# Kernel tuning notes

Hardware: AMD Instinct MI355X
Metric: run time of the kernel (lower is better)

Reference implementation:

```python
import jax, jax.numpy as jnp
import numpy as np

N, E = 50000, 800000
IN_DIM, HID, OUT_DIM = 128, 64, 64
H1, H2 = 4, 2
LRELU_SLOPE = 0.2
LN_EPS = 1e-5


def _glorot(key, shape):
    fan = shape[0] + shape[-1]
    lim = float(np.sqrt(6.0 / fan))
    return jax.random.uniform(key, shape, jnp.float32, -lim, lim)


def setup_inputs() -> dict:
    key = jax.random.key(0)
    ks = jax.random.split(key, 12)
    x = jax.random.normal(ks[0], (N, IN_DIM), jnp.float32)
    edge_index = jax.random.randint(ks[1], (2, E), 0, N, jnp.int64)
    return {
        "x": x,
        "edge_index": edge_index,
        # layer 1: GATConv(128 -> 64, heads=4, concat=True)
        "W1": _glorot(ks[2], (IN_DIM, H1 * HID)),
        "att_src1": _glorot(ks[3], (H1, HID)),
        "att_dst1": _glorot(ks[4], (H1, HID)),
        "b1": jnp.zeros((H1 * HID,), jnp.float32),
        # LayerNorm(256)
        "ln_w": jnp.ones((H1 * HID,), jnp.float32),
        "ln_b": jnp.zeros((H1 * HID,), jnp.float32),
        # layer 2: GATConv(256 -> 64, heads=2, concat=False)
        "W2": _glorot(ks[5], (H1 * HID, H2 * OUT_DIM)),
        "att_src2": _glorot(ks[6], (H2, OUT_DIM)),
        "att_dst2": _glorot(ks[7], (H2, OUT_DIM)),
        "b2": jnp.zeros((OUT_DIM,), jnp.float32),
    }


def gat_layer(x, src, dst, W, a_src, a_dst, bias, heads, out_ch, concat):
    n = x.shape[0]
    h = (x @ W).reshape(n, heads, out_ch)                 # [N,H,C]
    al_s = jnp.einsum("nhc,hc->nh", h, a_src)             # [N,H]
    al_d = jnp.einsum("nhc,hc->nh", h, a_dst)
    e = jax.nn.leaky_relu(al_s[src] + al_d[dst], LRELU_SLOPE)  # [E,H]
    # segment softmax over incoming edges of each dst node
    m = jax.ops.segment_max(e, dst, num_segments=n)
    e = jnp.exp(e - m[dst])
    denom = jax.ops.segment_sum(e, dst, num_segments=n)
    alpha = e / denom[dst]                                # [E,H]
    msg = h[src] * alpha[:, :, None]                      # [E,H,C]
    out = jax.ops.segment_sum(msg, dst, num_segments=n)   # [N,H,C]
    out = out.reshape(n, heads * out_ch) if concat else out.mean(axis=1)
    return out + bias


def layer_norm(x, w, b):
    mu = x.mean(axis=-1, keepdims=True)
    var = ((x - mu) ** 2).mean(axis=-1, keepdims=True)
    return (x - mu) * jax.lax.rsqrt(var + LN_EPS) * w + b


def reference(x, edge_index, W1, att_src1, att_dst1, b1, ln_w, ln_b,
              W2, att_src2, att_dst2, b2):
    # PyG GATConv adds self-loops by default
    loops = jnp.arange(N, dtype=edge_index.dtype)
    src = jnp.concatenate([edge_index[0], loops])
    dst = jnp.concatenate([edge_index[1], loops])
    h = gat_layer(x, src, dst, W1, att_src1, att_dst1, b1, H1, HID, True)
    h = layer_norm(h, ln_w, ln_b)
    h = jax.nn.elu(h)
    # dropout is identity in eval mode
    h = gat_layer(h, src, dst, W2, att_src2, att_dst2, b2, H2, OUT_DIM, False)
    return h
```

## Files before the change

### kernel.cpp

```cpp
#include <hip/hip_runtime.h>
#include <hip/hip_bf16.h>
#include <math.h>

#define IN_DIM  128
#define HID     64
#define H1      4
#define H2      2
#define OUT_DIM 64
#define D1      256
#define D2      128
#define LRELU   0.2f
#define LN_EPS  1e-5f
#define BK      16
#define NS      8
#define HKPS    49
#define MAXNB   4096

using short8 = __attribute__((ext_vector_type(8))) short;
using f32x4  = __attribute__((ext_vector_type(4))) float;

static __device__ __forceinline__ unsigned short f2bf_bits(float f)
{
    __hip_bfloat16 b = __float2bfloat16(f);
    return *reinterpret_cast<unsigned short*>(&b);
}
static __device__ __forceinline__ float2 unpack_bf2(unsigned int p)
{
    float2 r;
    r.x = __uint_as_float(p << 16);
    r.y = __uint_as_float(p & 0xffff0000u);
    return r;
}
static __device__ __forceinline__ unsigned int pack_bf2(float x, float y)
{
    return (unsigned int)f2bf_bits(x) | ((unsigned int)f2bf_bits(y) << 16);
}

static __device__ __forceinline__ float lrelu_exp(float v)
{
    v = v > 0.f ? v : LRELU * v;
    return __expf(v);
}

static __device__ __forceinline__ int detect_i64(const int* __restrict__ ei)
{
    int any_odd_nonzero = 0;
    #pragma unroll
    for (int k = 1; k < 16; k += 2) any_odd_nonzero |= (ei[k] != 0);
    return any_odd_nonzero ? 0 : 1;
}

__global__ __launch_bounds__(256) void conv_hist_kernel(
    const float* __restrict__ W1, const float* __restrict__ W2,
    unsigned short* __restrict__ Wp1, unsigned short* __restrict__ Wp2,
    const int* __restrict__ ei, int E, int* __restrict__ sdeg, int NB)
{
    __shared__ int hist[MAXNB];
    const int bid = blockIdx.x;
    if (bid < 256) {
        int tid = bid * 256 + threadIdx.x;
        if (tid < 32768) {
            int j = tid & 7, l = (tid >> 3) & 63, rest = tid >> 9;
            int s = rest & 15, t = rest >> 4;
            int k = t * 32 + (l >> 4) * 8 + j, col = s * 16 + (l & 15);
            Wp1[tid] = f2bf_bits(W1[k * D1 + col]);
        } else {
            int id = tid - 32768;
            int j = id & 7, l = (id >> 3) & 63, rest = id >> 9;
            int s = rest & 7, t = rest >> 3;
            int k = t * 32 + (l >> 4) * 8 + j, col = s * 16 + (l & 15);
            Wp2[id] = f2bf_bits(W2[k * D2 + col]);
        }
        return;
    }

    const int i64f = detect_i64(ei);
    const int h = bid - 256;
    const int s = h & 7, k = h >> 3;
    const int numGroups = (E + 255) >> 8;

    for (int i = threadIdx.x; i < NB; i += 256) hist[i] = 0;
    __syncthreads();

    for (int g = s + 8 * k; g < numGroups; g += 8 * HKPS) {
        int e = (g << 8) + threadIdx.x;
        if (e < E) {
            int dst = i64f ? ei[2 * ((size_t)E + e)] : ei[E + e];
            atomicAdd(&hist[dst >> 4], 1);
        }
    }
    __syncthreads();
    for (int i = threadIdx.x; i < NB; i += 256) {
        int v = hist[i];
        if (v) atomicAdd(&sdeg[s * NB + i], v);
    }
}

__global__ __launch_bounds__(256) void scan_gemm1_kernel(
    const int* __restrict__ sdeg, int NB, int M, int* __restrict__ bsum, int scanB,
    const float* __restrict__ x, const unsigned short* __restrict__ Wp,
    const float* __restrict__ att_s, const float* __restrict__ att_d,
    unsigned short* __restrict__ h1b,
    float* __restrict__ al_s, float* __restrict__ al_d, int N)
{
    __shared__ __align__(16) unsigned short As[16 * 136];
    const int tid = threadIdx.x;

    if ((int)blockIdx.x < scanB) {
        int* sh = (int*)As;
        int i = blockIdx.x * 256 + tid;
        int v = 0;
        if (i < M) v = sdeg[(i & 7) * NB + (i >> 3)];
        sh[tid] = v;
        __syncthreads();
        for (int st = 128; st > 0; st >>= 1) {
            if (tid < st) sh[tid] += sh[tid + st];
            __syncthreads();
        }
        if (tid == 0) bsum[blockIdx.x] = sh[0];
        return;
    }

    const int n0 = ((int)blockIdx.x - scanB) * 16;
    const int l = tid & 63, w = tid >> 6;

    #pragma unroll
    for (int it = 0; it < 2; ++it) {
        int ch = tid + it * 256;
        int r = ch >> 5, c4 = (ch & 31) * 4;
        int row = n0 + r;
        float4 v = (row < N) ? ((const float4*)x)[(size_t)row * 32 + (c4 >> 2)]
                             : make_float4(0.f, 0.f, 0.f, 0.f);
        ushort4 pk = make_ushort4(f2bf_bits(v.x), f2bf_bits(v.y),
                                  f2bf_bits(v.z), f2bf_bits(v.w));
        *(ushort4*)&As[r * 136 + c4] = pk;
    }

    short8 bfr[4][4];
    #pragma unroll
    for (int t = 0; t < 4; ++t)
        #pragma unroll
        for (int p = 0; p < 4; ++p)
            bfr[t][p] = ((const short8*)Wp)[(t * 16 + (w * 4 + p)) * 64 + l];

    __syncthreads();

    f32x4 acc[4] = {{0.f,0.f,0.f,0.f},{0.f,0.f,0.f,0.f},
                    {0.f,0.f,0.f,0.f},{0.f,0.f,0.f,0.f}};
    #pragma unroll
    for (int t = 0; t < 4; ++t) {
        short8 a = *(const short8*)&As[(l & 15) * 136 + t * 32 + (l >> 4) * 8];
        #pragma unroll
        for (int p = 0; p < 4; ++p)
            acc[p] = __builtin_amdgcn_mfma_f32_16x16x32_bf16(a, bfr[t][p], acc[p], 0, 0, 0);
    }

    const int colbase = w * 64 + (l & 15);
    const int rowbase = n0 + (l >> 4) * 4;
    #pragma unroll
    for (int p = 0; p < 4; ++p) {
        int col = colbase + p * 16;
        #pragma unroll
        for (int r = 0; r < 4; ++r) {
            int row = rowbase + r;
            if (row < N) h1b[(size_t)row * D1 + col] = f2bf_bits(acc[p][r]);
        }
    }

    float as_p[4], ad_p[4];
    #pragma unroll
    for (int p = 0; p < 4; ++p) {
        as_p[p] = att_s[colbase + p * 16];
        ad_p[p] = att_d[colbase + p * 16];
    }
    #pragma unroll
    for (int r = 0; r < 4; ++r) {
        float ps = acc[0][r] * as_p[0] + acc[1][r] * as_p[1]
                 + acc[2][r] * as_p[2] + acc[3][r] * as_p[3];
        float pd = acc[0][r] * ad_p[0] + acc[1][r] * ad_p[1]
                 + acc[2][r] * ad_p[2] + acc[3][r] * ad_p[3];
        #pragma unroll
        for (int off = 8; off > 0; off >>= 1) {
            ps += __shfl_down(ps, off);
            pd += __shfl_down(pd, off);
        }
        int row = rowbase + r;
        if ((l & 15) == 0 && row < N) {
            al_s[(size_t)row * H1 + w] = ps;
            al_d[(size_t)row * H1 + w] = pd;
        }
    }
}

__global__ __launch_bounds__(256) void scan_final(
    const int* __restrict__ sdeg, const int* __restrict__ bsum, int B, int M, int NB,
    int* __restrict__ start, int* __restrict__ bcur)
{
    __shared__ int sb[256];
    __shared__ int s[256];
    sb[threadIdx.x] = (threadIdx.x < B) ? bsum[threadIdx.x] : 0;
    __syncthreads();
    for (int st = 1; st < 256; st <<= 1) {
        int t = (threadIdx.x >= st) ? sb[threadIdx.x - st] : 0;
        __syncthreads();
        sb[threadIdx.x] += t;
        __syncthreads();
    }
    const int blockOff = (blockIdx.x == 0) ? 0 : sb[blockIdx.x - 1];

    int i = blockIdx.x * 256 + threadIdx.x;
    int v = (i < M) ? sdeg[(i & 7) * NB + (i >> 3)] : 0;
    s[threadIdx.x] = v;
    __syncthreads();
    for (int st = 1; st < 256; st <<= 1) {
        int t = (threadIdx.x >= st) ? s[threadIdx.x - st] : 0;
        __syncthreads();
        s[threadIdx.x] += t;
        __syncthreads();
    }
    int excl = s[threadIdx.x] - v + blockOff;
    if (i < M) {
        start[i] = excl;
        bcur[(i & 7) * NB + (i >> 3)] = excl;
    }
}

__global__ __launch_bounds__(256) void bucket_scatter(
    const int* __restrict__ ei, int E, int NB,
    int* __restrict__ bcur, unsigned int* __restrict__ pairs)
{
    const int i64f = detect_i64(ei);
    int e = blockIdx.x * 256 + threadIdx.x;
    if (e >= E) return;
    int src, dst;
    if (i64f) { src = ei[2 * (size_t)e]; dst = ei[2 * ((size_t)E + e)]; }
    else      { src = ei[e];             dst = ei[E + e]; }
    int s = (e >> 8) & 7;
    int pos = atomicAdd(&bcur[s * NB + (dst >> 4)], 1);
    pairs[pos] = ((unsigned int)src << 16) | (unsigned int)dst;
}

__global__ __launch_bounds__(256) void fill2_kernel(
    const unsigned int* __restrict__ pairs, const int* __restrict__ start,
    int N, int NB, int E,
    int* __restrict__ rowptr, int* __restrict__ csr_src)
{
    __shared__ int cnt[BK], cur[BK];
    __shared__ int stage[2048];
    const int b = blockIdx.x;
    const int t = threadIdx.x;
    const int base = start[b * 8];
    const int segend = (b + 1 < NB) ? start[(b + 1) * 8] : E;
    const int seglen = segend - base;

    if (t < BK) cnt[t] = 0;
    __syncthreads();
    for (int i = t; i < seglen; i += 256)
        atomicAdd(&cnt[pairs[base + i] & (BK - 1)], 1);
    __syncthreads();
    if (t == 0) {
        int run = 0;
        for (int j = 0; j < BK; ++j) {
            cur[j] = run;
            int node = b * BK + j;
            if (node < N) rowptr[node] = base + run;
            run += cnt[j];
        }
        if (b == NB - 1) rowptr[N] = E;
    }
    __syncthreads();

    if (seglen <= 2048) {
        for (int i = t; i < seglen; i += 256) {
            unsigned int p = pairs[base + i];
            int pos = atomicAdd(&cur[p & (BK - 1)], 1);
            stage[pos] = (int)(p >> 16);
        }
        __syncthreads();
        for (int i = t; i < seglen; i += 256)
            csr_src[base + i] = stage[i];
    } else {
        for (int i = t; i < seglen; i += 256) {
            unsigned int p = pairs[base + i];
            int pos = atomicAdd(&cur[p & (BK - 1)], 1);
            csr_src[base + pos] = (int)(p >> 16);
        }
    }
}

__global__ __launch_bounds__(256) void gemm2_mfma(
    const unsigned short* __restrict__ hmidb, const unsigned short* __restrict__ Wp,
    const float* __restrict__ att_s, const float* __restrict__ att_d,
    unsigned short* __restrict__ h2b,
    float* __restrict__ al_s, float* __restrict__ al_d, int N)
{
    __shared__ __align__(16) unsigned short As[16 * 264];
    __shared__ float psL[4][16], pdL[4][16];
    const int tid = threadIdx.x;
    const int n0 = blockIdx.x * 16;
    const int l = tid & 63, w = tid >> 6;

    const short8 zero8 = {0,0,0,0,0,0,0,0};
    #pragma unroll
    for (int it = 0; it < 2; ++it) {
        int ch = tid + it * 256;
        int r = ch >> 5, c8 = (ch & 31) * 8;
        int row = n0 + r;
        short8 v = (row < N) ? ((const short8*)hmidb)[(size_t)row * 32 + (ch & 31)] : zero8;
        *(short8*)&As[r * 264 + c8] = v;
    }

    short8 bfr[8][2];
    #pragma unroll
    for (int t = 0; t < 8; ++t)
        #pragma unroll
        for (int q = 0; q < 2; ++q)
            bfr[t][q] = ((const short8*)Wp)[(t * 8 + (w * 2 + q)) * 64 + l];

    __syncthreads();

    f32x4 acc[2] = {{0.f,0.f,0.f,0.f},{0.f,0.f,0.f,0.f}};
    #pragma unroll
    for (int t = 0; t < 8; ++t) {
        short8 a = *(const short8*)&As[(l & 15) * 264 + t * 32 + (l >> 4) * 8];
        #pragma unroll
        for (int q = 0; q < 2; ++q)
            acc[q] = __builtin_amdgcn_mfma_f32_16x16x32_bf16(a, bfr[t][q], acc[q], 0, 0, 0);
    }

    const int colbase = w * 32 + (l & 15);
    const int rowbase = n0 + (l >> 4) * 4;
    #pragma unroll
    for (int q = 0; q < 2; ++q) {
        int col = colbase + q * 16;
        #pragma unroll
        for (int r = 0; r < 4; ++r) {
            int row = rowbase + r;
            if (row < N) h2b[(size_t)row * D2 + col] = f2bf_bits(acc[q][r]);
        }
    }

    float as_q[2], ad_q[2];
    #pragma unroll
    for (int q = 0; q < 2; ++q) {
        as_q[q] = att_s[colbase + q * 16];
        ad_q[q] = att_d[colbase + q * 16];
    }
    #pragma unroll
    for (int r = 0; r < 4; ++r) {
        float ps = acc[0][r] * as_q[0] + acc[1][r] * as_q[1];
        float pd = acc[0][r] * ad_q[0] + acc[1][r] * ad_q[1];
        #pragma unroll
        for (int off = 8; off > 0; off >>= 1) {
            ps += __shfl_down(ps, off);
            pd += __shfl_down(pd, off);
        }
        if ((l & 15) == 0) {
            psL[w][(l >> 4) * 4 + r] = ps;
            pdL[w][(l >> 4) * 4 + r] = pd;
        }
    }
    __syncthreads();
    if (tid < 32) {
        int rl = tid & 15, hh = tid >> 4;
        int row = n0 + rl;
        if (row < N) {
            al_s[(size_t)row * H2 + hh] = psL[2*hh][rl] + psL[2*hh+1][rl];
            al_d[(size_t)row * H2 + hh] = pdL[2*hh][rl] + pdL[2*hh+1][rl];
        }
    }
}

__global__ __launch_bounds__(64) void agg1_kernel(
    const int* __restrict__ rowptr, const int* __restrict__ csr_src,
    const uint2* __restrict__ h1p,
    const float* __restrict__ al_s, const float* __restrict__ al_d,
    const float* __restrict__ b1,
    const float* __restrict__ ln_w, const float* __restrict__ ln_b,
    uint2* __restrict__ hmidp, int N)
{
    const int n = blockIdx.x;
    const int l = threadIdx.x;
    const int h = l >> 4;
    const float ad = al_d[(size_t)n * H1 + h];

    float a0[4] = {0.f,0.f,0.f,0.f}, a1[4] = {0.f,0.f,0.f,0.f};
    float a2[4] = {0.f,0.f,0.f,0.f}, a3[4] = {0.f,0.f,0.f,0.f};
    float dn0, dn1 = 0.f, dn2 = 0.f, dn3 = 0.f;

    {
        float w = lrelu_exp(al_s[(size_t)n * H1 + h] + ad);
        uint2 p = h1p[(size_t)n * 64 + l];
        float2 va = unpack_bf2(p.x), vb = unpack_bf2(p.y);
        a0[0] = w * va.x; a0[1] = w * va.y; a0[2] = w * vb.x; a0[3] = w * vb.y;
        dn0 = w;
    }

    const int beg = rowptr[n], end = rowptr[n + 1];
    int i = beg;

#define LOADI(k)  int s##k = csr_src[i + k];
#define LOADR(k)  uint2 p##k = h1p[(size_t)s##k * 64 + l]; \
                  float g##k = al_s[(size_t)s##k * H1 + h];
#define WACC(A, D, k) { float w = lrelu_exp(g##k + ad); \
                        float2 va = unpack_bf2(p##k.x), vb = unpack_bf2(p##k.y); \
                        A[0] += w * va.x; A[1] += w * va.y; \
                        A[2] += w * vb.x; A[3] += w * vb.y; D += w; }

    for (; i + 4 <= end; i += 4) {
        LOADI(0) LOADI(1) LOADI(2) LOADI(3)
        LOADR(0) LOADR(1) LOADR(2) LOADR(3)
        WACC(a0, dn0, 0) WACC(a1, dn1, 1) WACC(a2, dn2, 2) WACC(a3, dn3, 3)
    }
    for (; i < end; ++i) {
        LOADI(0) LOADR(0) WACC(a0, dn0, 0)
    }
#undef LOADI
#undef LOADR
#undef WACC

    const float inv = 1.f / ((dn0 + dn1) + (dn2 + dn3));
    float4 bb = ((const float4*)b1)[l];
    float v[4];
    v[0] = ((a0[0]+a1[0]) + (a2[0]+a3[0])) * inv + bb.x;
    v[1] = ((a0[1]+a1[1]) + (a2[1]+a3[1])) * inv + bb.y;
    v[2] = ((a0[2]+a1[2]) + (a2[2]+a3[2])) * inv + bb.z;
    v[3] = ((a0[3]+a1[3]) + (a2[3]+a3[3])) * inv + bb.w;

    float s  = (v[0]+v[1]) + (v[2]+v[3]);
    float s2 = (v[0]*v[0]+v[1]*v[1]) + (v[2]*v[2]+v[3]*v[3]);
    #pragma unroll
    for (int off = 32; off > 0; off >>= 1) {
        s  += __shfl_down(s,  off);
        s2 += __shfl_down(s2, off);
    }
    const float mu   = __shfl(s,  0) * (1.f / 256.f);
    const float ex2  = __shfl(s2, 0) * (1.f / 256.f);
    const float rstd = rsqrtf(ex2 - mu * mu + LN_EPS);
    float4 lw = ((const float4*)ln_w)[l];
    float4 lb = ((const float4*)ln_b)[l];
    float y0 = (v[0] - mu) * rstd * lw.x + lb.x;
    float y1 = (v[1] - mu) * rstd * lw.y + lb.y;
    float y2 = (v[2] - mu) * rstd * lw.z + lb.z;
    float y3 = (v[3] - mu) * rstd * lw.w + lb.w;
    y0 = y0 > 0.f ? y0 : (__expf(y0) - 1.f);
    y1 = y1 > 0.f ? y1 : (__expf(y1) - 1.f);
    y2 = y2 > 0.f ? y2 : (__expf(y2) - 1.f);
    y3 = y3 > 0.f ? y3 : (__expf(y3) - 1.f);
    uint2 outp;
    outp.x = pack_bf2(y0, y1);
    outp.y = pack_bf2(y2, y3);
    hmidp[(size_t)n * 64 + l] = outp;
}

__global__ __launch_bounds__(64) void agg2_kernel(
    const int* __restrict__ rowptr, const int* __restrict__ csr_src,
    const unsigned int* __restrict__ h2p,
    const float* __restrict__ al_s, const float* __restrict__ al_d,
    const float* __restrict__ b2,
    float* __restrict__ out, int N)
{
    const int n = blockIdx.x;
    const int l = threadIdx.x;
    const int h = l >> 5;
    const float ad = al_d[(size_t)n * H2 + h];

    float ax0, ay0, dn0;
    float ax1 = 0.f, ay1 = 0.f, dn1 = 0.f;
    float ax2 = 0.f, ay2 = 0.f, dn2 = 0.f;
    float ax3 = 0.f, ay3 = 0.f, dn3 = 0.f;
    {
        float w = lrelu_exp(al_s[(size_t)n * H2 + h] + ad);
        float2 hv = unpack_bf2(h2p[(size_t)n * 64 + l]);
        ax0 = w * hv.x; ay0 = w * hv.y; dn0 = w;
    }

    const int beg = rowptr[n], end = rowptr[n + 1];
    int i = beg;

#define LOADI(k)  int s##k = csr_src[i + k];
#define LOADR(k)  unsigned int p##k = h2p[(size_t)s##k * 64 + l]; \
                  float g##k = al_s[(size_t)s##k * H2 + h];
#define WACC(AX, AY, D, k) { float w = lrelu_exp(g##k + ad); \
                             float2 vv = unpack_bf2(p##k); \
                             AX += w * vv.x; AY += w * vv.y; D += w; }

    for (; i + 4 <= end; i += 4) {
        LOADI(0) LOADI(1) LOADI(2) LOADI(3)
        LOADR(0) LOADR(1) LOADR(2) LOADR(3)
        WACC(ax0, ay0, dn0, 0) WACC(ax1, ay1, dn1, 1)
        WACC(ax2, ay2, dn2, 2) WACC(ax3, ay3, dn3, 3)
    }
    for (; i < end; ++i) {
        LOADI(0) LOADR(0) WACC(ax0, ay0, dn0, 0)
    }
#undef LOADI
#undef LOADR
#undef WACC

    const float inv = 1.f / ((dn0 + dn1) + (dn2 + dn3));
    const float vx = ((ax0 + ax1) + (ax2 + ax3)) * inv;
    const float vy = ((ay0 + ay1) + (ay2 + ay3)) * inv;

    const float vx1 = __shfl(vx, l + 32);
    const float vy1 = __shfl(vy, l + 32);
    if (l < 32) {
        float2 bb = ((const float2*)b2)[l];
        float2 o;
        o.x = 0.5f * (vx + vx1) + bb.x;
        o.y = 0.5f * (vy + vy1) + bb.y;
        ((float2*)out)[(size_t)n * 32 + l] = o;
    }
}

extern "C" void kernel_launch(void* const* d_in, const int* in_sizes, int n_in,
                              void* d_out, int out_size, void* d_ws, size_t ws_size,
                              hipStream_t stream)
{
    const float* x   = (const float*)d_in[0];
    const int*   ei  = (const int*)d_in[1];
    const float* W1  = (const float*)d_in[2];
    const float* as1 = (const float*)d_in[3];
    const float* ad1 = (const float*)d_in[4];
    const float* b1  = (const float*)d_in[5];
    const float* lnw = (const float*)d_in[6];
    const float* lnb = (const float*)d_in[7];
    const float* W2  = (const float*)d_in[8];
    const float* as2 = (const float*)d_in[9];
    const float* ad2 = (const float*)d_in[10];
    const float* b2  = (const float*)d_in[11];

    const int N = in_sizes[0] / IN_DIM;
    const int E = in_sizes[1] / 2;
    const int NB = (N + BK - 1) / BK;
    const int M  = NB * NS;

    char* ws = (char*)d_ws;
    const size_t szH1b = (size_t)N * D1 * sizeof(unsigned short);
    unsigned short* h1b   = (unsigned short*)(ws);
    unsigned short* hmidb = (unsigned short*)(ws + szH1b);
    unsigned short* Wp1   = (unsigned short*)(ws + 2 * szH1b);
    unsigned short* Wp2   = Wp1 + 32768;
    float* al_s1 = (float*)(Wp2 + 32768);
    float* al_d1 = al_s1 + (size_t)N * H1;
    float* al_s2 = al_d1 + (size_t)N * H1;
    float* al_d2 = al_s2 + (size_t)N * H2;
    int* sdeg    = (int*)(al_d2 + (size_t)N * H2);
    int* bcur    = sdeg + M;
    int* start   = bcur + M;
    int* rowptr  = start + M;
    int* csr_src = rowptr + (N + 1);
    int* bsum    = csr_src + E;
    unsigned int* pairs = (unsigned int*)(bsum + 256);
    unsigned short* h2b = h1b;

    hipMemsetAsync(sdeg, 0, (size_t)M * sizeof(int), stream);

    const int edgeBlocks = (E + 255) / 256;
    const int scanBlocks = (M + 255) / 256;
    const int tileBlocks = (N + 15) / 16;

    conv_hist_kernel<<<256 + NS * HKPS, 256, 0, stream>>>(W1, W2, Wp1, Wp2, ei, E, sdeg, NB);
    scan_gemm1_kernel<<<scanBlocks + tileBlocks, 256, 0, stream>>>(
        sdeg, NB, M, bsum, scanBlocks, x, Wp1, as1, ad1, h1b, al_s1, al_d1, N);
    scan_final<<<scanBlocks, 256, 0, stream>>>(sdeg, bsum, scanBlocks, M, NB, start, bcur);
    bucket_scatter<<<edgeBlocks, 256, 0, stream>>>(ei, E, NB, bcur, pairs);
    fill2_kernel<<<NB, 256, 0, stream>>>(pairs, start, N, NB, E, rowptr, csr_src);

    agg1_kernel<<<N, 64, 0, stream>>>(rowptr, csr_src, (const uint2*)h1b,
                                      al_s1, al_d1, b1, lnw, lnb,
                                      (uint2*)hmidb, N);
    gemm2_mfma<<<tileBlocks, 256, 0, stream>>>(hmidb, Wp2, as2, ad2, h2b, al_s2, al_d2, N);
    agg2_kernel<<<N, 64, 0, stream>>>(rowptr, csr_src, (const unsigned int*)h2b,
                                      al_s2, al_d2, b2, (float*)d_out, N);
}
```

Before: 275.0 us.

## Use 64 per-block histogram slices with direct stores instead of atomics

The dst histogram now gives each of 64 blocks its own slice, written with plain stores. This removes the global atomics and the memset of sdeg. The bucket scatter spreads edges over 64 sub-slices, which cuts atomic contention on the bucket cursors. The scan and final scan are reworked for the larger M: block offsets are now computed by reducing the preceding block sums instead of a 256-entry scan. The cost is a larger M to scan, and only 64 blocks reading all edges during the histogram phase, which may be underparallel.

```diff
diff --git a/kernel.cpp b/kernel.cpp
--- a/kernel.cpp
+++ b/kernel.cpp
@@ -12,8 +12,7 @@
 #define LRELU   0.2f
 #define LN_EPS  1e-5f
 #define BK      16
-#define NS      8
-#define HKPS    49
+#define NSS     64
 #define MAXNB   4096
 
 using short8 = __attribute__((ext_vector_type(8))) short;
@@ -75,14 +74,13 @@
     }
 
     const int i64f = detect_i64(ei);
-    const int h = bid - 256;
-    const int s = h & 7, k = h >> 3;
+    const int s = bid - 256;
     const int numGroups = (E + 255) >> 8;
 
     for (int i = threadIdx.x; i < NB; i += 256) hist[i] = 0;
     __syncthreads();
 
-    for (int g = s + 8 * k; g < numGroups; g += 8 * HKPS) {
+    for (int g = s; g < numGroups; g += NSS) {
         int e = (g << 8) + threadIdx.x;
         if (e < E) {
             int dst = i64f ? ei[2 * ((size_t)E + e)] : ei[E + e];
@@ -90,10 +88,8 @@
         }
     }
     __syncthreads();
-    for (int i = threadIdx.x; i < NB; i += 256) {
-        int v = hist[i];
-        if (v) atomicAdd(&sdeg[s * NB + i], v);
-    }
+    for (int i = threadIdx.x; i < NB; i += 256)
+        sdeg[s * NB + i] = hist[i];
 }
 
 __global__ __launch_bounds__(256) void scan_gemm1_kernel(
@@ -110,7 +106,7 @@
         int* sh = (int*)As;
         int i = blockIdx.x * 256 + tid;
         int v = 0;
-        if (i < M) v = sdeg[(i & 7) * NB + (i >> 3)];
+        if (i < M) v = sdeg[(i & 63) * NB + (i >> 6)];
         sh[tid] = v;
         __syncthreads();
         for (int st = 128; st > 0; st >>= 1) {
@@ -193,23 +189,23 @@
 }
 
 __global__ __launch_bounds__(256) void scan_final(
-    const int* __restrict__ sdeg, const int* __restrict__ bsum, int B, int M, int NB,
+    const int* __restrict__ sdeg, const int* __restrict__ bsum, int M, int NB,
     int* __restrict__ start, int* __restrict__ bcur)
 {
-    __shared__ int sb[256];
+    __shared__ int red[256];
     __shared__ int s[256];
-    sb[threadIdx.x] = (threadIdx.x < B) ? bsum[threadIdx.x] : 0;
-    __syncthreads();
-    for (int st = 1; st < 256; st <<= 1) {
-        int t = (threadIdx.x >= st) ? sb[threadIdx.x - st] : 0;
+    int part = 0;
+    for (int j = threadIdx.x; j < (int)blockIdx.x; j += 256) part += bsum[j];
+    red[threadIdx.x] = part;
+    __syncthreads();
+    for (int st = 128; st > 0; st >>= 1) {
+        if (threadIdx.x < st) red[threadIdx.x] += red[threadIdx.x + st];
         __syncthreads();
-        sb[threadIdx.x] += t;
-        __syncthreads();
-    }
-    const int blockOff = (blockIdx.x == 0) ? 0 : sb[blockIdx.x - 1];
+    }
+    const int blockOff = red[0];
 
     int i = blockIdx.x * 256 + threadIdx.x;
-    int v = (i < M) ? sdeg[(i & 7) * NB + (i >> 3)] : 0;
+    int v = (i < M) ? sdeg[(i & 63) * NB + (i >> 6)] : 0;
     s[threadIdx.x] = v;
     __syncthreads();
     for (int st = 1; st < 256; st <<= 1) {
@@ -221,7 +217,7 @@
     int excl = s[threadIdx.x] - v + blockOff;
     if (i < M) {
         start[i] = excl;
-        bcur[(i & 7) * NB + (i >> 3)] = excl;
+        bcur[(i & 63) * NB + (i >> 6)] = excl;
     }
 }
 
@@ -235,7 +231,7 @@
     int src, dst;
     if (i64f) { src = ei[2 * (size_t)e]; dst = ei[2 * ((size_t)E + e)]; }
     else      { src = ei[e];             dst = ei[E + e]; }
-    int s = (e >> 8) & 7;
+    int s = (e >> 8) & 63;
     int pos = atomicAdd(&bcur[s * NB + (dst >> 4)], 1);
     pairs[pos] = ((unsigned int)src << 16) | (unsigned int)dst;
 }
@@ -249,8 +245,8 @@
     __shared__ int stage[2048];
     const int b = blockIdx.x;
     const int t = threadIdx.x;
-    const int base = start[b * 8];
-    const int segend = (b + 1 < NB) ? start[(b + 1) * 8] : E;
+    const int base = start[b * NSS];
+    const int segend = (b + 1 < NB) ? start[(b + 1) * NSS] : E;
     const int seglen = segend - base;
 
     if (t < BK) cnt[t] = 0;
@@ -533,7 +529,7 @@
     const int N = in_sizes[0] / IN_DIM;
     const int E = in_sizes[1] / 2;
     const int NB = (N + BK - 1) / BK;
-    const int M  = NB * NS;
+    const int M  = NB * NSS;
 
     char* ws = (char*)d_ws;
     const size_t szH1b = (size_t)N * D1 * sizeof(unsigned short);
@@ -551,19 +547,17 @@
     int* rowptr  = start + M;
     int* csr_src = rowptr + (N + 1);
     int* bsum    = csr_src + E;
-    unsigned int* pairs = (unsigned int*)(bsum + 256);
+    unsigned int* pairs = (unsigned int*)(bsum + 1024);
     unsigned short* h2b = h1b;
-
-    hipMemsetAsync(sdeg, 0, (size_t)M * sizeof(int), stream);
 
     const int edgeBlocks = (E + 255) / 256;
     const int scanBlocks = (M + 255) / 256;
     const int tileBlocks = (N + 15) / 16;
 
-    conv_hist_kernel<<<256 + NS * HKPS, 256, 0, stream>>>(W1, W2, Wp1, Wp2, ei, E, sdeg, NB);
+    conv_hist_kernel<<<256 + NSS, 256, 0, stream>>>(W1, W2, Wp1, Wp2, ei, E, sdeg, NB);
     scan_gemm1_kernel<<<scanBlocks + tileBlocks, 256, 0, stream>>>(
         sdeg, NB, M, bsum, scanBlocks, x, Wp1, as1, ad1, h1b, al_s1, al_d1, N);
-    scan_final<<<scanBlocks, 256, 0, stream>>>(sdeg, bsum, scanBlocks, M, NB, start, bcur);
+    scan_final<<<scanBlocks, 256, 0, stream>>>(sdeg, bsum, M, NB, start, bcur);
     bucket_scatter<<<edgeBlocks, 256, 0, stream>>>(ei, E, NB, bcur, pairs);
     fill2_kernel<<<NB, 256, 0, stream>>>(pairs, start, N, NB, E, rowptr, csr_src);
 
```

Result: slower. 285.6 us (+3.8%).

## Fuse CSR fill with layer-1 aggregation, reading neighbor lists from shared memory

Applied to the files above, without the earlier changes.

The CSR bucket fill and the layer-1 attention aggregation now run in one kernel. After building each 16-node bucket's sorted source list in shared memory, the block's four waves each aggregate four nodes straight from that staged list. This removes one kernel launch and the global re-read of rowptr and csr_src for layer 1. In exchange, each block is serialized over 16 nodes with only 4 waves, which could lower parallelism and latency hiding compared with the previous one-wave-per-node grid.

```diff
diff --git a/kernel.cpp b/kernel.cpp
--- a/kernel.cpp
+++ b/kernel.cpp
@@ -240,147 +240,14 @@
     pairs[pos] = ((unsigned int)src << 16) | (unsigned int)dst;
 }
 
-__global__ __launch_bounds__(256) void fill2_kernel(
-    const unsigned int* __restrict__ pairs, const int* __restrict__ start,
-    int N, int NB, int E,
-    int* __restrict__ rowptr, int* __restrict__ csr_src)
-{
-    __shared__ int cnt[BK], cur[BK];
-    __shared__ int stage[2048];
-    const int b = blockIdx.x;
-    const int t = threadIdx.x;
-    const int base = start[b * 8];
-    const int segend = (b + 1 < NB) ? start[(b + 1) * 8] : E;
-    const int seglen = segend - base;
-
-    if (t < BK) cnt[t] = 0;
-    __syncthreads();
-    for (int i = t; i < seglen; i += 256)
-        atomicAdd(&cnt[pairs[base + i] & (BK - 1)], 1);
-    __syncthreads();
-    if (t == 0) {
-        int run = 0;
-        for (int j = 0; j < BK; ++j) {
-            cur[j] = run;
-            int node = b * BK + j;
-            if (node < N) rowptr[node] = base + run;
-            run += cnt[j];
-        }
-        if (b == NB - 1) rowptr[N] = E;
-    }
-    __syncthreads();
-
-    if (seglen <= 2048) {
-        for (int i = t; i < seglen; i += 256) {
-            unsigned int p = pairs[base + i];
-            int pos = atomicAdd(&cur[p & (BK - 1)], 1);
-            stage[pos] = (int)(p >> 16);
-        }
-        __syncthreads();
-        for (int i = t; i < seglen; i += 256)
-            csr_src[base + i] = stage[i];
-    } else {
-        for (int i = t; i < seglen; i += 256) {
-            unsigned int p = pairs[base + i];
-            int pos = atomicAdd(&cur[p & (BK - 1)], 1);
-            csr_src[base + pos] = (int)(p >> 16);
-        }
-    }
-}
-
-__global__ __launch_bounds__(256) void gemm2_mfma(
-    const unsigned short* __restrict__ hmidb, const unsigned short* __restrict__ Wp,
-    const float* __restrict__ att_s, const float* __restrict__ att_d,
-    unsigned short* __restrict__ h2b,
-    float* __restrict__ al_s, float* __restrict__ al_d, int N)
-{
-    __shared__ __align__(16) unsigned short As[16 * 264];
-    __shared__ float psL[4][16], pdL[4][16];
-    const int tid = threadIdx.x;
-    const int n0 = blockIdx.x * 16;
-    const int l = tid & 63, w = tid >> 6;
-
-    const short8 zero8 = {0,0,0,0,0,0,0,0};
-    #pragma unroll
-    for (int it = 0; it < 2; ++it) {
-        int ch = tid + it * 256;
-        int r = ch >> 5, c8 = (ch & 31) * 8;
-        int row = n0 + r;
-        short8 v = (row < N) ? ((const short8*)hmidb)[(size_t)row * 32 + (ch & 31)] : zero8;
-        *(short8*)&As[r * 264 + c8] = v;
-    }
-
-    short8 bfr[8][2];
-    #pragma unroll
-    for (int t = 0; t < 8; ++t)
-        #pragma unroll
-        for (int q = 0; q < 2; ++q)
-            bfr[t][q] = ((const short8*)Wp)[(t * 8 + (w * 2 + q)) * 64 + l];
-
-    __syncthreads();
-
-    f32x4 acc[2] = {{0.f,0.f,0.f,0.f},{0.f,0.f,0.f,0.f}};
-    #pragma unroll
-    for (int t = 0; t < 8; ++t) {
-        short8 a = *(const short8*)&As[(l & 15) * 264 + t * 32 + (l >> 4) * 8];
-        #pragma unroll
-        for (int q = 0; q < 2; ++q)
-            acc[q] = __builtin_amdgcn_mfma_f32_16x16x32_bf16(a, bfr[t][q], acc[q], 0, 0, 0);
-    }
-
-    const int colbase = w * 32 + (l & 15);
-    const int rowbase = n0 + (l >> 4) * 4;
-    #pragma unroll
-    for (int q = 0; q < 2; ++q) {
-        int col = colbase + q * 16;
-        #pragma unroll
-        for (int r = 0; r < 4; ++r) {
-            int row = rowbase + r;
-            if (row < N) h2b[(size_t)row * D2 + col] = f2bf_bits(acc[q][r]);
-        }
-    }
-
-    float as_q[2], ad_q[2];
-    #pragma unroll
-    for (int q = 0; q < 2; ++q) {
-        as_q[q] = att_s[colbase + q * 16];
-        ad_q[q] = att_d[colbase + q * 16];
-    }
-    #pragma unroll
-    for (int r = 0; r < 4; ++r) {
-        float ps = acc[0][r] * as_q[0] + acc[1][r] * as_q[1];
-        float pd = acc[0][r] * ad_q[0] + acc[1][r] * ad_q[1];
-        #pragma unroll
-        for (int off = 8; off > 0; off >>= 1) {
-            ps += __shfl_down(ps, off);
-            pd += __shfl_down(pd, off);
-        }
-        if ((l & 15) == 0) {
-            psL[w][(l >> 4) * 4 + r] = ps;
-            pdL[w][(l >> 4) * 4 + r] = pd;
-        }
-    }
-    __syncthreads();
-    if (tid < 32) {
-        int rl = tid & 15, hh = tid >> 4;
-        int row = n0 + rl;
-        if (row < N) {
-            al_s[(size_t)row * H2 + hh] = psL[2*hh][rl] + psL[2*hh+1][rl];
-            al_d[(size_t)row * H2 + hh] = pdL[2*hh][rl] + pdL[2*hh+1][rl];
-        }
-    }
-}
-
-__global__ __launch_bounds__(64) void agg1_kernel(
-    const int* __restrict__ rowptr, const int* __restrict__ csr_src,
+static __device__ __forceinline__ void agg1_node(
+    int n, int l, const int* __restrict__ srcidx, int ec,
     const uint2* __restrict__ h1p,
     const float* __restrict__ al_s, const float* __restrict__ al_d,
     const float* __restrict__ b1,
     const float* __restrict__ ln_w, const float* __restrict__ ln_b,
-    uint2* __restrict__ hmidp, int N)
-{
-    const int n = blockIdx.x;
-    const int l = threadIdx.x;
+    uint2* __restrict__ hmidp)
+{
     const int h = l >> 4;
     const float ad = al_d[(size_t)n * H1 + h];
 
@@ -396,23 +263,20 @@
         dn0 = w;
     }
 
-    const int beg = rowptr[n], end = rowptr[n + 1];
-    int i = beg;
-
-#define LOADI(k)  int s##k = csr_src[i + k];
+    int i = 0;
+#define LOADI(k)  int s##k = srcidx[i + k];
 #define LOADR(k)  uint2 p##k = h1p[(size_t)s##k * 64 + l]; \
                   float g##k = al_s[(size_t)s##k * H1 + h];
 #define WACC(A, D, k) { float w = lrelu_exp(g##k + ad); \
                         float2 va = unpack_bf2(p##k.x), vb = unpack_bf2(p##k.y); \
                         A[0] += w * va.x; A[1] += w * va.y; \
                         A[2] += w * vb.x; A[3] += w * vb.y; D += w; }
-
-    for (; i + 4 <= end; i += 4) {
+    for (; i + 4 <= ec; i += 4) {
         LOADI(0) LOADI(1) LOADI(2) LOADI(3)
         LOADR(0) LOADR(1) LOADR(2) LOADR(3)
         WACC(a0, dn0, 0) WACC(a1, dn1, 1) WACC(a2, dn2, 2) WACC(a3, dn3, 3)
     }
-    for (; i < end; ++i) {
+    for (; i < ec; ++i) {
         LOADI(0) LOADR(0) WACC(a0, dn0, 0)
     }
 #undef LOADI
@@ -451,6 +315,155 @@
     outp.x = pack_bf2(y0, y1);
     outp.y = pack_bf2(y2, y3);
     hmidp[(size_t)n * 64 + l] = outp;
+}
+
+__global__ __launch_bounds__(256) void fill_agg1_kernel(
+    const unsigned int* __restrict__ pairs, const int* __restrict__ start,
+    const uint2* __restrict__ h1p,
+    const float* __restrict__ al_s, const float* __restrict__ al_d,
+    const float* __restrict__ b1,
+    const float* __restrict__ ln_w, const float* __restrict__ ln_b,
+    int N, int NB, int E,
+    int* __restrict__ rowptr, int* __restrict__ csr_src,
+    uint2* __restrict__ hmidp)
+{
+    __shared__ int cnt[BK], cur[BK], cur0[BK];
+    __shared__ int stage[2048];
+    const int b = blockIdx.x;
+    const int t = threadIdx.x;
+    const int base = start[b * NS];
+    const int segend = (b + 1 < NB) ? start[(b + 1) * NS] : E;
+    const int seglen = segend - base;
+    const bool fits = (seglen <= 2048);
+
+    if (t < BK) cnt[t] = 0;
+    __syncthreads();
+    for (int i = t; i < seglen; i += 256)
+        atomicAdd(&cnt[pairs[base + i] & (BK - 1)], 1);
+    __syncthreads();
+    if (t == 0) {
+        int run = 0;
+        for (int j = 0; j < BK; ++j) {
+            cur[j] = run; cur0[j] = run;
+            int node = b * BK + j;
+            if (node < N) rowptr[node] = base + run;
+            run += cnt[j];
+        }
+        if (b == NB - 1) rowptr[N] = E;
+    }
+    __syncthreads();
+
+    if (fits) {
+        for (int i = t; i < seglen; i += 256) {
+            unsigned int p = pairs[base + i];
+            int pos = atomicAdd(&cur[p & (BK - 1)], 1);
+            stage[pos] = (int)(p >> 16);
+        }
+        __syncthreads();
+        for (int i = t; i < seglen; i += 256)
+            csr_src[base + i] = stage[i];
+    } else {
+        for (int i = t; i < seglen; i += 256) {
+            unsigned int p = pairs[base + i];
+            int pos = atomicAdd(&cur[p & (BK - 1)], 1);
+            csr_src[base + pos] = (int)(p >> 16);
+        }
+    }
+    __syncthreads();
+
+    const int l = t & 63, w = t >> 6;
+    #pragma unroll
+    for (int r = 0; r < 4; ++r) {
+        int j = w * 4 + r;
+        int n = b * BK + j;
+        if (n >= N) break;
+        const int* srcidx = fits ? ((const int*)stage + cur0[j])
+                                 : (csr_src + base + cur0[j]);
+        agg1_node(n, l, srcidx, cnt[j], h1p, al_s, al_d, b1, ln_w, ln_b, hmidp);
+    }
+}
+
+__global__ __launch_bounds__(256) void gemm2_mfma(
+    const unsigned short* __restrict__ hmidb, const unsigned short* __restrict__ Wp,
+    const float* __restrict__ att_s, const float* __restrict__ att_d,
+    unsigned short* __restrict__ h2b,
+    float* __restrict__ al_s, float* __restrict__ al_d, int N)
+{
+    __shared__ __align__(16) unsigned short As[16 * 264];
+    __shared__ float psL[4][16], pdL[4][16];
+    const int tid = threadIdx.x;
+    const int n0 = blockIdx.x * 16;
+    const int l = tid & 63, w = tid >> 6;
+
+    const short8 zero8 = {0,0,0,0,0,0,0,0};
+    #pragma unroll
+    for (int it = 0; it < 2; ++it) {
+        int ch = tid + it * 256;
+        int r = ch >> 5, c8 = (ch & 31) * 8;
+        int row = n0 + r;
+        short8 v = (row < N) ? ((const short8*)hmidb)[(size_t)row * 32 + (ch & 31)] : zero8;
+        *(short8*)&As[r * 264 + c8] = v;
+    }
+
+    short8 bfr[8][2];
+    #pragma unroll
+    for (int t = 0; t < 8; ++t)
+        #pragma unroll
+        for (int q = 0; q < 2; ++q)
+            bfr[t][q] = ((const short8*)Wp)[(t * 8 + (w * 2 + q)) * 64 + l];
+
+    __syncthreads();
+
+    f32x4 acc[2] = {{0.f,0.f,0.f,0.f},{0.f,0.f,0.f,0.f}};
+    #pragma unroll
+    for (int t = 0; t < 8; ++t) {
+        short8 a = *(const short8*)&As[(l & 15) * 264 + t * 32 + (l >> 4) * 8];
+        #pragma unroll
+        for (int q = 0; q < 2; ++q)
+            acc[q] = __builtin_amdgcn_mfma_f32_16x16x32_bf16(a, bfr[t][q], acc[q], 0, 0, 0);
+    }
+
+    const int colbase = w * 32 + (l & 15);
+    const int rowbase = n0 + (l >> 4) * 4;
+    #pragma unroll
+    for (int q = 0; q < 2; ++q) {
+        int col = colbase + q * 16;
+        #pragma unroll
+        for (int r = 0; r < 4; ++r) {
+            int row = rowbase + r;
+            if (row < N) h2b[(size_t)row * D2 + col] = f2bf_bits(acc[q][r]);
+        }
+    }
+
+    float as_q[2], ad_q[2];
+    #pragma unroll
+    for (int q = 0; q < 2; ++q) {
+        as_q[q] = att_s[colbase + q * 16];
+        ad_q[q] = att_d[colbase + q * 16];
+    }
+    #pragma unroll
+    for (int r = 0; r < 4; ++r) {
+        float ps = acc[0][r] * as_q[0] + acc[1][r] * as_q[1];
+        float pd = acc[0][r] * ad_q[0] + acc[1][r] * ad_q[1];
+        #pragma unroll
+        for (int off = 8; off > 0; off >>= 1) {
+            ps += __shfl_down(ps, off);
+            pd += __shfl_down(pd, off);
+        }
+        if ((l & 15) == 0) {
+            psL[w][(l >> 4) * 4 + r] = ps;
+            pdL[w][(l >> 4) * 4 + r] = pd;
+        }
+    }
+    __syncthreads();
+    if (tid < 32) {
+        int rl = tid & 15, hh = tid >> 4;
+        int row = n0 + rl;
+        if (row < N) {
+            al_s[(size_t)row * H2 + hh] = psL[2*hh][rl] + psL[2*hh+1][rl];
+            al_d[(size_t)row * H2 + hh] = pdL[2*hh][rl] + pdL[2*hh+1][rl];
+        }
+    }
 }
 
 __global__ __launch_bounds__(64) void agg2_kernel(
@@ -565,11 +578,10 @@
         sdeg, NB, M, bsum, scanBlocks, x, Wp1, as1, ad1, h1b, al_s1, al_d1, N);
     scan_final<<<scanBlocks, 256, 0, stream>>>(sdeg, bsum, scanBlocks, M, NB, start, bcur);
     bucket_scatter<<<edgeBlocks, 256, 0, stream>>>(ei, E, NB, bcur, pairs);
-    fill2_kernel<<<NB, 256, 0, stream>>>(pairs, start, N, NB, E, rowptr, csr_src);
-
-    agg1_kernel<<<N, 64, 0, stream>>>(rowptr, csr_src, (const uint2*)h1b,
-                                      al_s1, al_d1, b1, lnw, lnb,
-                                      (uint2*)hmidb, N);
+    fill_agg1_kernel<<<NB, 256, 0, stream>>>(pairs, start, (const uint2*)h1b,
+                                             al_s1, al_d1, b1, lnw, lnb,
+                                             N, NB, E, rowptr, csr_src,
+                                             (uint2*)hmidb);
     gemm2_mfma<<<tileBlocks, 256, 0, stream>>>(hmidb, Wp2, as2, ad2, h2b, al_s2, al_d2, N);
     agg2_kernel<<<N, 64, 0, stream>>>(rowptr, csr_src, (const unsigned int*)h2b,
                                       al_s2, al_d2, b2, (float*)d_out, N);
```

Measured after the change: 278.9 us. About the same (+1.4%).
